# Optimization experiments

Hardware: AMD Instinct MI355X
Metric: run time of the kernel (lower is better)

Reference implementation:

```python
import jax, jax.numpy as jnp
import numpy as np

B, N, DPOS, F, P, K = 32, 1024, 3, 64, 128, 16


def setup_inputs() -> dict:
    key = jax.random.key(0)
    kp, kf, kw1, kw2 = jax.random.split(key, 4)
    points = jax.random.normal(kp, (B, N, DPOS), dtype=jnp.float32)
    features = jax.random.normal(kf, (B, N, F), dtype=jnp.float32)
    W1 = jax.random.normal(kw1, (2 * F, 2 * P), dtype=jnp.float32) * (1.0 / np.sqrt(2 * F))
    b1 = jnp.zeros((2 * P,), dtype=jnp.float32)
    W2 = jax.random.normal(kw2, (2 * P, P), dtype=jnp.float32) * (1.0 / np.sqrt(2 * P))
    b2 = jnp.zeros((P,), dtype=jnp.float32)
    return {"points": points, "features": features, "W1": W1, "b1": b1, "W2": W2, "b2": b2}


def reference(points, features, W1, b1, W2, b2):
    # pairwise squared distances: r_i - 2 p_i.p_j + r_j + 1e-5  -> [B, N, N]
    r = jnp.sum(points * points, axis=2, keepdims=True)
    m = jnp.einsum('bnd,bmd->bnm', points, points)
    D = r - 2.0 * m + jnp.swapaxes(r, 1, 2) + 1e-5
    # K+1 nearest (incl. self), drop self -> indices [B, N, K]
    _, idx = jax.lax.top_k(-D, K + 1)
    idx = idx[:, :, 1:]
    # gather neighbor features: [B, N, K, F]
    neighbors = features[jnp.arange(B)[:, None, None], idx]
    center = jnp.broadcast_to(features[:, :, None, :], neighbors.shape)
    local = jnp.concatenate([neighbors - center, center], axis=-1)  # [B,N,K,2F]
    # 2-layer MLP with exact GELU
    h = jax.nn.gelu(jnp.einsum('bnkf,fh->bnkh', local, W1) + b1, approximate=False)
    out = jax.nn.gelu(jnp.einsum('bnkh,hp->bnkp', h, W2) + b2, approximate=False)
    # mean over neighbors -> [B, N, P]
    return jnp.mean(out, axis=2)
```

## Files before the change

kernel.cpp:

```cpp
#include <hip/hip_runtime.h>
#include <math.h>

#define BB 32
#define NN 1024
#define FF 64
#define PP 128
#define KNN 16
#define H2 256
#define F2 128
#define KSEL 17
#define SVCAP 272

typedef float f32x4 __attribute__((ext_vector_type(4)));
typedef __bf16 bf16x8 __attribute__((ext_vector_type(8)));

__device__ __forceinline__ float gelu_fast(float x) {
    float s = x * x;
    float arg = x * fmaf(s, -0.1029438f, -2.3022115f);
    float e = __builtin_amdgcn_exp2f(arg);
    return x * __builtin_amdgcn_rcpf(1.0f + e);
}

__global__ __launch_bounds__(512, 8) void knn_prep(const float* __restrict__ points,
                                                   int* __restrict__ idx_out,
                                                   const float* __restrict__ W1,
                                                   const float* __restrict__ W2,
                                                   __bf16* __restrict__ Wcf,
                                                   __bf16* __restrict__ W2f) {
    if (blockIdx.x >= 4096) {
        int tid = (blockIdx.x - 4096) * 512 + threadIdx.x;
        if (tid < 4096) {
            const int lane = tid & 63, quad = lane >> 4, l16 = lane & 15;
            const int kk = (tid >> 6) & 1, n_tile = tid >> 7;
            const int n = n_tile * 16 + l16;
            const int kb = kk * 32 + quad * 8;
            bf16x8 v;
#pragma unroll
            for (int j = 0; j < 8; ++j) {
                const int k = kb + j;
                float x = (n < 256) ? W1[k * 256 + n]
                                    : (W1[(64 + k) * 256 + (n - 256)] - W1[k * 256 + (n - 256)]);
                v[j] = (__bf16)x;
            }
            *(bf16x8*)(Wcf + (size_t)tid * 8) = v;
        } else {
            const int t2 = tid - 4096;
            const int lane = t2 & 63, quad = lane >> 4, l16 = lane & 15;
            const int nt = (t2 >> 6) & 7, kk8 = t2 >> 9;
            const int p = nt * 16 + l16;
            const int hb = kk8 * 32 + quad * 8;
            bf16x8 v;
#pragma unroll
            for (int j = 0; j < 8; ++j) v[j] = (__bf16)W2[(size_t)(hb + j) * PP + p];
            *(bf16x8*)(W2f + (size_t)t2 * 8) = v;
        }
        return;
    }

    __shared__ float4 pts[NN];
    __shared__ unsigned sv_val[8][SVCAP];
    __shared__ unsigned sv_idx[8][SVCAP];
    __shared__ unsigned tie_idx[8][64];

    const int t = threadIdx.x;
    const int w = t >> 6, lane = t & 63;
    const int b = blockIdx.x >> 7;
    const int q0 = (blockIdx.x & 127) * 8;
    const float* pb = points + (size_t)b * NN * 3;
    const unsigned long long lt = (1ull << lane) - 1ull;

    for (int i = t; i < NN; i += 512) {
        float x = pb[3 * i], y = pb[3 * i + 1], z = pb[3 * i + 2];
        float r = __fadd_rn(__fadd_rn(__fmul_rn(x, x), __fmul_rn(y, y)), __fmul_rn(z, z));
        pts[i] = make_float4(x, y, z, r);
    }
    __syncthreads();

    const int qn = q0 + w;
    const int gq = b * NN + qn;
    const float4 qp = pts[qn];

    float D[16];
#pragma unroll
    for (int j = 0; j < 16; ++j) {
        float4 c = pts[j * 64 + lane];
        float dot = __fadd_rn(__fadd_rn(__fmul_rn(qp.x, c.x), __fmul_rn(qp.y, c.y)),
                              __fmul_rn(qp.z, c.z));
        D[j] = __fadd_rn(__fadd_rn(__fsub_rn(qp.w, __fmul_rn(2.0f, dot)), c.w), 1e-5f);
    }

    float mnf = D[0];
#pragma unroll
    for (int j = 1; j < 16; ++j) mnf = fminf(mnf, D[j]);
    const unsigned mbits = __float_as_uint(mnf);

    unsigned T = 0;
#pragma unroll
    for (int bit = 31; bit >= 0; --bit) {
        unsigned cand = T | (1u << bit);
        int cnt = __popcll(__ballot(mbits < cand));
        if (cnt < KSEL) T = cand;
    }

    unsigned base = 0;
#pragma unroll
    for (int j = 0; j < 16; ++j) {
        unsigned vb = __float_as_uint(D[j]);
        bool keep = (vb <= T);
        unsigned long long m = __ballot(keep);
        if (keep) {
            unsigned pos = base + (unsigned)__popcll(m & lt);
            if (pos < SVCAP) { sv_val[w][pos] = vb; sv_idx[w][pos] = j * 64 + lane; }
        }
        base += (unsigned)__popcll(m);
    }
    unsigned C = base > SVCAP ? SVCAP : base;
    const int S = (int)((C + 63) >> 6);

    unsigned Ts = 0;
    if (S == 1) {
        unsigned xv0 = (lane < (int)C) ? sv_val[w][lane] : 0xFFFFFFFFu;
#pragma unroll
        for (int bit = 31; bit >= 0; --bit) {
            unsigned cand = Ts | (1u << bit);
            int cnt = __popcll(__ballot(xv0 < cand));
            if (cnt < KSEL) Ts = cand;
        }
    } else {
        for (int bit = 31; bit >= 0; --bit) {
            unsigned cand = Ts | (1u << bit);
            int cnt = 0;
            for (int s = 0; s < S; ++s) {
                int i = s * 64 + lane;
                unsigned vb = (i < (int)C) ? sv_val[w][i] : 0xFFFFFFFFu;
                cnt += __popcll(__ballot(vb < cand));
            }
            if (cnt < KSEL) Ts = cand;
        }
    }

    int L = 0;
    for (int s = 0; s < S; ++s) {
        int i = s * 64 + lane;
        unsigned vb = (i < (int)C) ? sv_val[w][i] : 0xFFFFFFFFu;
        L += __popcll(__ballot(vb < Ts));
    }
    const int need = KSEL - L;

    unsigned vmin_l = 0xFFFFFFFFu;
    for (int s = 0; s < S; ++s) {
        int i = s * 64 + lane;
        unsigned vb = (i < (int)C) ? sv_val[w][i] : 0xFFFFFFFFu;
        vmin_l = vmin_l < vb ? vmin_l : vb;
    }
#pragma unroll
    for (int off = 32; off >= 1; off >>= 1) {
        unsigned o2 = __shfl_xor(vmin_l, off, 64);
        vmin_l = vmin_l < o2 ? vmin_l : o2;
    }
    const unsigned Vmin = vmin_l;
    unsigned imin_l = 0xFFFFFFFFu;
    for (int s = 0; s < S; ++s) {
        int i = s * 64 + lane;
        unsigned vb = (i < (int)C) ? sv_val[w][i] : 0xFFFFFFFFu;
        unsigned mi = (i < (int)C) ? sv_idx[w][i] : 0xFFFFFFFFu;
        if (vb == Vmin && mi < imin_l) imin_l = mi;
    }
#pragma unroll
    for (int off = 32; off >= 1; off >>= 1) {
        unsigned o2 = __shfl_xor(imin_l, off, 64);
        imin_l = imin_l < o2 ? imin_l : o2;
    }
    const unsigned dropIdx = imin_l;

    int* o = idx_out + (size_t)gq * KNN;
    unsigned wbase = 0, tbase = 0;
    for (int s = 0; s < S; ++s) {
        int i = s * 64 + lane;
        unsigned vb = (i < (int)C) ? sv_val[w][i] : 0xFFFFFFFFu;
        unsigned mi = (i < (int)C) ? sv_idx[w][i] : 0xFFFFFFFFu;
        bool wk = (vb < Ts) && (mi != dropIdx);
        unsigned long long wm = __ballot(wk);
        if (wk) o[wbase + (unsigned)__popcll(wm & lt)] = (int)mi;
        wbase += (unsigned)__popcll(wm);
        bool tk = (vb == Ts);
        unsigned long long tm2 = __ballot(tk);
        if (tk) {
            unsigned tp = tbase + (unsigned)__popcll(tm2 & lt);
            if (tp < 64) tie_idx[w][tp] = mi;
        }
        tbase += (unsigned)__popcll(tm2);
    }
    unsigned tc = tbase > 64 ? 64 : tbase;
    if ((int)tc == need) {
        bool tk = (lane < (int)tc);
        unsigned mi2 = tk ? tie_idx[w][lane] : 0xFFFFFFFFu;
        tk = tk && (mi2 != dropIdx);
        unsigned long long m3 = __ballot(tk);
        if (tk) o[wbase + (unsigned)__popcll(m3 & lt)] = (int)mi2;
    } else if (lane == 0) {
        unsigned pos = wbase;
        for (int r = 0; r < need; ++r) {
            unsigned best = 0xFFFFFFFFu; int bj = 0;
            for (int j2 = 0; j2 < (int)tc; ++j2) {
                unsigned mi = tie_idx[w][j2];
                if (mi < best) { best = mi; bj = j2; }
            }
            tie_idx[w][bj] = 0xFFFFFFFFu;
            if (best != dropIdx) o[pos++] = (int)best;
        }
    }
}

__global__ __launch_bounds__(256, 4) void gq_gemm(const float* __restrict__ feat,
                                                  const __bf16* __restrict__ Wcf,
                                                  const float* __restrict__ b1,
                                                  __bf16* __restrict__ Gall,
                                                  __bf16* __restrict__ Qall) {
    __shared__ __align__(16) __bf16 st[4][16][136];
    const int t = threadIdx.x, w = t >> 6, lane = t & 63;
    const int quad = lane >> 4, l16 = lane & 15;
    const int m0 = blockIdx.x * 16;

    bf16x8 a[2];
#pragma unroll
    for (int kk = 0; kk < 2; ++kk) {
        const float* ap = feat + (size_t)(m0 + l16) * 64 + kk * 32 + quad * 8;
        float4 a0 = *(const float4*)ap, a1 = *(const float4*)(ap + 4);
        bf16x8 v;
        v[0] = (__bf16)a0.x; v[1] = (__bf16)a0.y; v[2] = (__bf16)a0.z; v[3] = (__bf16)a0.w;
        v[4] = (__bf16)a1.x; v[5] = (__bf16)a1.y; v[6] = (__bf16)a1.z; v[7] = (__bf16)a1.w;
        a[kk] = v;
    }
    f32x4 acc[8];
#pragma unroll
    for (int nt = 0; nt < 8; ++nt) acc[nt] = (f32x4){0.f, 0.f, 0.f, 0.f};
#pragma unroll
    for (int kk = 0; kk < 2; ++kk)
#pragma unroll
        for (int nt = 0; nt < 8; ++nt) {
            bf16x8 bf = *(const bf16x8*)(Wcf + (size_t)(((w * 8 + nt) * 2 + kk) * 64 + lane) * 8);
            acc[nt] = __builtin_amdgcn_mfma_f32_16x16x32_bf16(a[kk], bf, acc[nt], 0, 0, 0);
        }

    const bool isQ = (w >= 2);
#pragma unroll
    for (int nt = 0; nt < 8; ++nt) {
        const int col = nt * 16 + l16;
        const float bias = isQ ? b1[(w - 2) * 128 + col] : 0.f;
#pragma unroll
        for (int r = 0; r < 4; ++r)
            st[w][quad * 4 + r][col] = (__bf16)(acc[nt][r] + bias);
    }
    __syncthreads();

    const int row = lane >> 2, c = lane & 3;
    const int m = m0 + row;
#pragma unroll
    for (int i = 0; i < 4; ++i) {
        const int col = c * 32 + i * 8;
        bf16x8 v = *(const bf16x8*)&st[w][row][col];
        if (!isQ) *(bf16x8*)(Gall + (size_t)m * H2 + w * 128 + col) = v;
        else      *(bf16x8*)(Qall + (size_t)m * H2 + (w - 2) * 128 + col) = v;
    }
}

__global__ __launch_bounds__(512, 4) void fused_mlp6(const __bf16* __restrict__ Gall,
                                                     const __bf16* __restrict__ Qall,
                                                     const int* __restrict__ knn_idx,
                                                     const __bf16* __restrict__ W2f,
                                                     const float* __restrict__ b2,
                                                     float* __restrict__ out) {
    __shared__ __align__(16) __bf16 w2s[16384];
    const int t = threadIdx.x, w = t >> 6, lane = t & 63;
    const int quad = lane >> 4, l16 = lane & 15;

    const int wave_id = blockIdx.x * 8 + w;
    const int q0 = wave_id * 2;
    const int b = q0 >> 10;
    const int nb0 = knn_idx[q0 * KNN + l16];
    const int nb1 = knn_idx[(q0 + 1) * KNN + l16];
    const __bf16* g0 = Gall + ((size_t)(b << 10) + nb0) * H2;
    const __bf16* g1 = Gall + ((size_t)(b << 10) + nb1) * H2;
    const __bf16* qq0 = Qall + (size_t)q0 * H2;
    const __bf16* qq1 = qq0 + H2;

    f32x4 acc[2][8];
#pragma unroll
    for (int tm = 0; tm < 2; ++tm)
#pragma unroll
        for (int nt = 0; nt < 8; ++nt) acc[tm][nt] = (f32x4){0.f, 0.f, 0.f, 0.f};

#pragma unroll
    for (int half = 0; half < 2; ++half) {
        if (half) __syncthreads();
#pragma unroll
        for (int i = 0; i < 4; ++i) {
            bf16x8 v = *(const bf16x8*)(W2f + (size_t)(half * 2048 + i * 512 + t) * 8);
            *(bf16x8*)&w2s[(size_t)(i * 512 + t) * 8] = v;
        }
        __syncthreads();

#pragma unroll
        for (int kl = 0; kl < 4; ++kl) {
            const int ho = (half * 4 + kl) * 32 + quad * 8;
            bf16x8 gA = *(const bf16x8*)(g0 + ho);
            bf16x8 qA = *(const bf16x8*)(qq0 + ho);
            bf16x8 gB = *(const bf16x8*)(g1 + ho);
            bf16x8 qB = *(const bf16x8*)(qq1 + ho);
            bf16x8 a0, a1;
#pragma unroll
            for (int j = 0; j < 8; ++j) {
                a0[j] = (__bf16)gelu_fast((float)gA[j] + (float)qA[j]);
                a1[j] = (__bf16)gelu_fast((float)gB[j] + (float)qB[j]);
            }
            const __bf16* bb = &w2s[(kl * 8) * 512 + lane * 8];
#pragma unroll
            for (int nt = 0; nt < 8; ++nt) {
                bf16x8 bf = *(const bf16x8*)(bb + nt * 512);
                acc[0][nt] = __builtin_amdgcn_mfma_f32_16x16x32_bf16(a0, bf, acc[0][nt], 0, 0, 0);
                acc[1][nt] = __builtin_amdgcn_mfma_f32_16x16x32_bf16(a1, bf, acc[1][nt], 0, 0, 0);
            }
        }
    }

#pragma unroll
    for (int tm = 0; tm < 2; ++tm)
#pragma unroll
        for (int nt = 0; nt < 8; ++nt) {
            const float bias = b2[nt * 16 + l16];
            float s = 0.f;
#pragma unroll
            for (int r = 0; r < 4; ++r) s += gelu_fast(acc[tm][nt][r] + bias);
            s += __shfl_xor(s, 16, 64);
            s += __shfl_xor(s, 32, 64);
            if (quad == 0)
                out[(size_t)(q0 + tm) * PP + nt * 16 + l16] = s * 0.0625f;
        }
}

extern "C" void kernel_launch(void* const* d_in, const int* in_sizes, int n_in,
                              void* d_out, int out_size, void* d_ws, size_t ws_size,
                              hipStream_t stream) {
    const float* points   = (const float*)d_in[0];
    const float* features = (const float*)d_in[1];
    const float* W1 = (const float*)d_in[2];
    const float* b1 = (const float*)d_in[3];
    const float* W2 = (const float*)d_in[4];
    const float* b2 = (const float*)d_in[5];
    float* out = (float*)d_out;

    const size_t IDX_B  = (size_t)BB * NN * KNN * 4;
    const size_t WCF_B  = 512 * 64 * 2;
    const size_t W2F_B  = 256 * 128 * 2;
    const size_t G_B    = (size_t)BB * NN * H2 * 2;

    int* knn_idx = (int*)d_ws;
    char* p = (char*)d_ws + IDX_B;
    __bf16* Wcf  = (__bf16*)p;  p += WCF_B;
    __bf16* W2f  = (__bf16*)p;  p += W2F_B;
    __bf16* Gall = (__bf16*)p;  p += G_B;
    __bf16* Qall = (__bf16*)p;

    knn_prep<<<4112, 512, 0, stream>>>(points, knn_idx, W1, W2, Wcf, W2f);
    gq_gemm<<<2048, 256, 0, stream>>>(features, Wcf, b1, Gall, Qall);
    fused_mlp6<<<2048, 512, 0, stream>>>(Gall, Qall, knn_idx, W2f, b2, out);
}
```

Baseline: 213.8 us.

## Split point storage into SoA, shorten radix threshold search, shrink MLP blocks

The kNN kernel now keeps point coordinates as separate float arrays in shared memory, and its threshold search covers only the top 16 bits of the minimum distances, padding the low bits with ones. This roughly halves the serial ballot loop, but the candidate set may grow and hit the SVCAP cap more often. The fused MLP kernel moves to 256-thread blocks with half the shared W2 staging and processes W2 in four quarters. That gives more, smaller blocks with lower LDS use per block, at the cost of more barriers.

```diff
diff --git a/kernel.cpp b/kernel.cpp
--- a/kernel.cpp
+++ b/kernel.cpp
@@ -57,7 +57,7 @@
         return;
     }
 
-    __shared__ float4 pts[NN];
+    __shared__ float px[NN], py[NN], pz[NN], rr[NN];
     __shared__ unsigned sv_val[8][SVCAP];
     __shared__ unsigned sv_idx[8][SVCAP];
     __shared__ unsigned tie_idx[8][64];
@@ -71,22 +71,22 @@
 
     for (int i = t; i < NN; i += 512) {
         float x = pb[3 * i], y = pb[3 * i + 1], z = pb[3 * i + 2];
-        float r = __fadd_rn(__fadd_rn(__fmul_rn(x, x), __fmul_rn(y, y)), __fmul_rn(z, z));
-        pts[i] = make_float4(x, y, z, r);
+        px[i] = x; py[i] = y; pz[i] = z;
+        rr[i] = __fadd_rn(__fadd_rn(__fmul_rn(x, x), __fmul_rn(y, y)), __fmul_rn(z, z));
     }
     __syncthreads();
 
     const int qn = q0 + w;
     const int gq = b * NN + qn;
-    const float4 qp = pts[qn];
+    const float qx = px[qn], qy = py[qn], qz = pz[qn], qw = rr[qn];
 
     float D[16];
 #pragma unroll
     for (int j = 0; j < 16; ++j) {
-        float4 c = pts[j * 64 + lane];
-        float dot = __fadd_rn(__fadd_rn(__fmul_rn(qp.x, c.x), __fmul_rn(qp.y, c.y)),
-                              __fmul_rn(qp.z, c.z));
-        D[j] = __fadd_rn(__fadd_rn(__fsub_rn(qp.w, __fmul_rn(2.0f, dot)), c.w), 1e-5f);
+        const int m = j * 64 + lane;
+        float dot = __fadd_rn(__fadd_rn(__fmul_rn(qx, px[m]), __fmul_rn(qy, py[m])),
+                              __fmul_rn(qz, pz[m]));
+        D[j] = __fadd_rn(__fadd_rn(__fsub_rn(qw, __fmul_rn(2.0f, dot)), rr[m]), 1e-5f);
     }
 
     float mnf = D[0];
@@ -94,13 +94,15 @@
     for (int j = 1; j < 16; ++j) mnf = fminf(mnf, D[j]);
     const unsigned mbits = __float_as_uint(mnf);
 
-    unsigned T = 0;
-#pragma unroll
-    for (int bit = 31; bit >= 0; --bit) {
-        unsigned cand = T | (1u << bit);
-        int cnt = __popcll(__ballot(mbits < cand));
-        if (cnt < KSEL) T = cand;
-    }
+    const unsigned mhi = mbits >> 16;
+    unsigned Thi = 0;
+#pragma unroll
+    for (int bit = 15; bit >= 0; --bit) {
+        unsigned cand = Thi | (1u << bit);
+        int cnt = __popcll(__ballot(mhi < cand));
+        if (cnt < KSEL) Thi = cand;
+    }
+    const unsigned T = (Thi << 16) | 0xFFFFu;
 
     unsigned base = 0;
 #pragma unroll
@@ -265,17 +267,17 @@
     }
 }
 
-__global__ __launch_bounds__(512, 4) void fused_mlp6(const __bf16* __restrict__ Gall,
+__global__ __launch_bounds__(256, 4) void fused_mlp7(const __bf16* __restrict__ Gall,
                                                      const __bf16* __restrict__ Qall,
                                                      const int* __restrict__ knn_idx,
                                                      const __bf16* __restrict__ W2f,
                                                      const float* __restrict__ b2,
                                                      float* __restrict__ out) {
-    __shared__ __align__(16) __bf16 w2s[16384];
+    __shared__ __align__(16) __bf16 w2s[8192];
     const int t = threadIdx.x, w = t >> 6, lane = t & 63;
     const int quad = lane >> 4, l16 = lane & 15;
 
-    const int wave_id = blockIdx.x * 8 + w;
+    const int wave_id = blockIdx.x * 4 + w;
     const int q0 = wave_id * 2;
     const int b = q0 >> 10;
     const int nb0 = knn_idx[q0 * KNN + l16];
@@ -292,18 +294,18 @@
         for (int nt = 0; nt < 8; ++nt) acc[tm][nt] = (f32x4){0.f, 0.f, 0.f, 0.f};
 
 #pragma unroll
-    for (int half = 0; half < 2; ++half) {
-        if (half) __syncthreads();
+    for (int qtr = 0; qtr < 4; ++qtr) {
+        if (qtr) __syncthreads();
 #pragma unroll
         for (int i = 0; i < 4; ++i) {
-            bf16x8 v = *(const bf16x8*)(W2f + (size_t)(half * 2048 + i * 512 + t) * 8);
-            *(bf16x8*)&w2s[(size_t)(i * 512 + t) * 8] = v;
+            bf16x8 v = *(const bf16x8*)(W2f + (size_t)(qtr * 8192 + i * 2048 + t * 8));
+            *(bf16x8*)&w2s[i * 2048 + t * 8] = v;
         }
         __syncthreads();
 
 #pragma unroll
-        for (int kl = 0; kl < 4; ++kl) {
-            const int ho = (half * 4 + kl) * 32 + quad * 8;
+        for (int kl = 0; kl < 2; ++kl) {
+            const int ho = (qtr * 2 + kl) * 32 + quad * 8;
             bf16x8 gA = *(const bf16x8*)(g0 + ho);
             bf16x8 qA = *(const bf16x8*)(qq0 + ho);
             bf16x8 gB = *(const bf16x8*)(g1 + ho);
@@ -314,7 +316,7 @@
                 a0[j] = (__bf16)gelu_fast((float)gA[j] + (float)qA[j]);
                 a1[j] = (__bf16)gelu_fast((float)gB[j] + (float)qB[j]);
             }
-            const __bf16* bb = &w2s[(kl * 8) * 512 + lane * 8];
+            const __bf16* bb = &w2s[kl * 4096 + lane * 8];
 #pragma unroll
             for (int nt = 0; nt < 8; ++nt) {
                 bf16x8 bf = *(const bf16x8*)(bb + nt * 512);
@@ -364,5 +366,5 @@
 
     knn_prep<<<4112, 512, 0, stream>>>(points, knn_idx, W1, W2, Wcf, W2f);
     gq_gemm<<<2048, 256, 0, stream>>>(features, Wcf, b1, Gall, Qall);
-    fused_mlp6<<<2048, 512, 0, stream>>>(Gall, Qall, knn_idx, W2f, b2, out);
-}
+    fused_mlp7<<<4096, 256, 0, stream>>>(Gall, Qall, knn_idx, W2f, b2, out);
+}
```

New measurement: 205.9 us. 3.7% less time.
